# Kernel tuning notes

Measured on AMD Instinct MI355X. Metric: run time of the kernel, lower is better.

Reference implementation:

```python
import jax, jax.numpy as jnp
import numpy as np
from jax import lax

DIM = 256
HEADS = 8
C3 = DIM * 3 // 4  # 192
C1 = DIM // 4      # 64


def conv1x1(x, w):
    # x: [b,c,h,w], w: [o,c] (1x1 conv, no bias)
    return jnp.einsum('bchw,oc->bohw', x, w)


def dwconv3x3(x, w):
    # x: [b,c,h,w], w: [c,1,3,3] depthwise
    return lax.conv_general_dilated(
        x, w, window_strides=(1, 1), padding='SAME',
        feature_group_count=x.shape[1],
        dimension_numbers=('NCHW', 'OIHW', 'NCHW'))


def l2norm(x, eps=1e-12):
    # torch F.normalize: x / max(||x||, eps) along last dim
    n = jnp.sqrt(jnp.sum(x * x, axis=-1, keepdims=True))
    return x / jnp.maximum(n, eps)


def setup_inputs() -> dict:
    key = jax.random.key(0)
    ks = jax.random.split(key, 10)
    s = 0.02
    return {
        'x': jax.random.normal(ks[0], (4, DIM, 128, 128), jnp.float32),
        'k_v': jax.random.normal(ks[1], (4, 256), jnp.float32),
        'temperature': jnp.ones((HEADS, 1, 1), jnp.float32),
        'w_kR': jax.random.normal(ks[2], (C3, 192), jnp.float32) * s,
        'w_kI': jax.random.normal(ks[3], (C1, 64), jnp.float32) * s,
        'w_qR': jax.random.normal(ks[4], (DIM, C3), jnp.float32) * s,
        'w_qdw': jax.random.normal(ks[5], (DIM, 1, 3, 3), jnp.float32) * s,
        'w_kvI': jax.random.normal(ks[6], (2 * DIM, C1), jnp.float32) * s,
        'w_kvdw': jax.random.normal(ks[7], (2 * DIM, 1, 3, 3), jnp.float32) * s,
        'w_proj': jax.random.normal(ks[8], (DIM, DIM), jnp.float32) * s,
    }


def reference(x, k_v, temperature, w_kR, w_kI, w_qR, w_qdw, w_kvI, w_kvdw, w_proj):
    b, c, h, w = x.shape
    # FiLM-style modulation: x * kv + x
    kvr = (k_v[:, :192] @ w_kR.T)[:, :, None, None]  # [b, C3, 1, 1]
    kvi = (k_v[:, 192:] @ w_kI.T)[:, :, None, None]  # [b, C1, 1, 1]
    x_r = x[:, :C3] * kvr + x[:, :C3]
    x_i = x[:, C3:] * kvi + x[:, C3:]
    # QKV projections
    q = dwconv3x3(conv1x1(x_r, w_qR), w_qdw)          # [b, dim, h, w]
    kv = dwconv3x3(conv1x1(x_i, w_kvI), w_kvdw)       # [b, 2*dim, h, w]
    k, v = jnp.split(kv, 2, axis=1)
    hd = DIM // HEADS
    hw = h * w
    q = q.reshape(b, HEADS, hd, hw)
    k = k.reshape(b, HEADS, hd, hw)
    v = v.reshape(b, HEADS, hd, hw)
    # channel-wise (transposed) attention with L2 norm + temperature
    q = l2norm(q)
    k = l2norm(k)
    attn = jnp.einsum('bhcn,bhdn->bhcd', q, k) * temperature  # [b,H,hd,hd]
    attn = jax.nn.softmax(attn, axis=-1)
    out = jnp.einsum('bhcd,bhdn->bhcn', attn, v)
    out = out.reshape(b, DIM, h, w)
    return conv1x1(out, w_proj)
```

## Files before the change

kernel.cpp:

```cpp
#include <hip/hip_runtime.h>
#include <math.h>

#define HW 16384

typedef unsigned int uint;
typedef short bfrag __attribute__((ext_vector_type(8)));
typedef float f32x4 __attribute__((ext_vector_type(4)));

union FragCvt { uint4 u; bfrag v; };

__device__ inline uint pack2bf(float a, float b) {
  uint ua = __builtin_bit_cast(uint, a);
  uint ub = __builtin_bit_cast(uint, b);
  ua = (ua + 0x7FFFu + ((ua >> 16) & 1u)) >> 16;
  ub = (ub + 0x7FFFu + ((ub >> 16) & 1u)) & 0xFFFF0000u;
  return ua | ub;
}

__device__ inline void cvt_hilo(float4 a, float4 b, bfrag& hi, bfrag& lo) {
  float v0[8] = {a.x, a.y, a.z, a.w, b.x, b.y, b.z, b.w};
  uint hv[4], lv[4];
  #pragma unroll
  for (int i = 0; i < 4; ++i) {
    float x0 = v0[2 * i], x1 = v0[2 * i + 1];
    uint h = pack2bf(x0, x1);
    float h0 = __builtin_bit_cast(float, h << 16);
    float h1 = __builtin_bit_cast(float, h & 0xFFFF0000u);
    hv[i] = h;
    lv[i] = pack2bf(x0 - h0, x1 - h1);
  }
  FragCvt ch, cl;
  ch.u = make_uint4(hv[0], hv[1], hv[2], hv[3]);
  cl.u = make_uint4(lv[0], lv[1], lv[2], lv[3]);
  hi = ch.v;
  lo = cl.v;
}

__global__ __launch_bounds__(256) void mod_kernel(
    const float* __restrict__ kv, const float* __restrict__ wkR,
    const float* __restrict__ wkI, float* __restrict__ mod)
{
  int b = blockIdx.x;
  int c = threadIdx.x;
  const float* kvb = kv + b * 256;
  float s = 0.f;
  if (c < 192) {
    const float* wr = wkR + c * 192;
    for (int j = 0; j < 192; ++j) s += kvb[j] * wr[j];
  } else {
    const float* wi = wkI + (c - 192) * 64;
    for (int j = 0; j < 64; ++j) s += kvb[192 + j] * wi[j];
  }
  mod[b * 256 + c] = 1.f + s;
}

__global__ __launch_bounds__(256) void mgemm(
    const float* __restrict__ W, int ldW, size_t Wbstride,
    const float* __restrict__ X, int c0, size_t Xbstride,
    const float* __restrict__ mod,
    float* __restrict__ Y, size_t Ybstride, int K)
{
  int b = blockIdx.z, mt = blockIdx.y, nt = blockIdx.x;
  const float* Wb = W + (size_t)b * Wbstride + (size_t)mt * 128 * ldW;
  const float* Xb = X + (size_t)b * Xbstride + (size_t)c0 * HW + nt * 128;
  float* Yb = Y + (size_t)b * Ybstride + (size_t)mt * 128 * HW + nt * 128;

  __shared__ unsigned short Al[128 * 40];
  __shared__ unsigned short Bl[128 * 40];

  int t = threadIdx.x;
  int w = t >> 6, l = t & 63;
  int wm = (w >> 1) * 64, wn = (w & 1) * 64;
  int lm = l & 15, lk = (l >> 4) * 8;

  int am = t >> 1, ako = (t & 1) * 16;
  int bn = t & 127, bo = (t >> 7) * 8;

  f32x4 acc[4][4];
  #pragma unroll
  for (int fi = 0; fi < 4; ++fi)
    #pragma unroll
    for (int fj = 0; fj < 4; ++fj) acc[fi][fj] = {0.f, 0.f, 0.f, 0.f};

  for (int k0 = 0; k0 < K; k0 += 32) {
    const float* wsrc = Wb + (size_t)am * ldW + k0 + ako;
    float4 a0 = *(const float4*)(wsrc);
    float4 a1 = *(const float4*)(wsrc + 4);
    float4 a2 = *(const float4*)(wsrc + 8);
    float4 a3 = *(const float4*)(wsrc + 12);

    float xr[2][8];
    #pragma unroll
    for (int i = 0; i < 2; ++i) {
      int kb = k0 + bo + i * 16;
      #pragma unroll
      for (int r = 0; r < 8; ++r)
        xr[i][r] = Xb[(size_t)(kb + r) * HW + bn];
    }
    float sc[2][8];
    if (mod) {
      const float* mp = mod + b * 256 + c0 + k0 + bo;
      #pragma unroll
      for (int i = 0; i < 2; ++i) {
        float4 m0 = *(const float4*)(mp + i * 16);
        float4 m1 = *(const float4*)(mp + i * 16 + 4);
        sc[i][0] = m0.x; sc[i][1] = m0.y; sc[i][2] = m0.z; sc[i][3] = m0.w;
        sc[i][4] = m1.x; sc[i][5] = m1.y; sc[i][6] = m1.z; sc[i][7] = m1.w;
      }
    } else {
      #pragma unroll
      for (int i = 0; i < 2; ++i)
        #pragma unroll
        for (int r = 0; r < 8; ++r) sc[i][r] = 1.f;
    }

    __syncthreads();

    uint4 aw0, aw1;
    aw0.x = pack2bf(a0.x, a0.y); aw0.y = pack2bf(a0.z, a0.w);
    aw0.z = pack2bf(a1.x, a1.y); aw0.w = pack2bf(a1.z, a1.w);
    aw1.x = pack2bf(a2.x, a2.y); aw1.y = pack2bf(a2.z, a2.w);
    aw1.z = pack2bf(a3.x, a3.y); aw1.w = pack2bf(a3.z, a3.w);
    *(uint4*)&Al[am * 40 + ako] = aw0;
    *(uint4*)&Al[am * 40 + ako + 8] = aw1;

    #pragma unroll
    for (int i = 0; i < 2; ++i) {
      uint4 bw;
      bw.x = pack2bf(xr[i][0] * sc[i][0], xr[i][1] * sc[i][1]);
      bw.y = pack2bf(xr[i][2] * sc[i][2], xr[i][3] * sc[i][3]);
      bw.z = pack2bf(xr[i][4] * sc[i][4], xr[i][5] * sc[i][5]);
      bw.w = pack2bf(xr[i][6] * sc[i][6], xr[i][7] * sc[i][7]);
      *(uint4*)&Bl[bn * 40 + bo + i * 16] = bw;
    }

    __syncthreads();

    bfrag af[4], bfr[4];
    #pragma unroll
    for (int fj = 0; fj < 4; ++fj) {
      FragCvt cv;
      cv.u = *(const uint4*)&Al[(wm + fj * 16 + lm) * 40 + lk];
      af[fj] = cv.v;
    }
    #pragma unroll
    for (int fi = 0; fi < 4; ++fi) {
      FragCvt cv;
      cv.u = *(const uint4*)&Bl[(wn + fi * 16 + lm) * 40 + lk];
      bfr[fi] = cv.v;
    }
    #pragma unroll
    for (int fi = 0; fi < 4; ++fi)
      #pragma unroll
      for (int fj = 0; fj < 4; ++fj)
        acc[fi][fj] = __builtin_amdgcn_mfma_f32_16x16x32_bf16(
            bfr[fi], af[fj], acc[fi][fj], 0, 0, 0);
  }

  int ph = (l >> 4) * 4;
  #pragma unroll
  for (int fi = 0; fi < 4; ++fi)
    #pragma unroll
    for (int fj = 0; fj < 4; ++fj)
      *(f32x4*)&Yb[(size_t)(wm + fj * 16 + lm) * HW + wn + fi * 16 + ph] =
          acc[fi][fj];
}

__global__ __launch_bounds__(256) void dwconv_kernel(
    const float* __restrict__ in, size_t in_bstride,
    const float* __restrict__ wdw,
    float* __restrict__ out, size_t out_bstride,
    float* __restrict__ ssq)
{
  int c = blockIdx.x;
  int b = blockIdx.y;
  int t = threadIdx.x;
  int r = t >> 5;
  int xq = t & 31;

  const float4* ip4 = (const float4*)(in + (size_t)b * in_bstride + ((size_t)c << 14));
  float4* op4 = (float4*)(out + (size_t)b * out_bstride + ((size_t)c << 14));
  const float* wp = wdw + c * 9;
  float w0 = wp[0], w1 = wp[1], w2 = wp[2], w3 = wp[3], w4 = wp[4],
        w5 = wp[5], w6 = wp[6], w7 = wp[7], w8 = wp[8];

  const float4 z4 = make_float4(0.f, 0.f, 0.f, 0.f);
  int y0 = r << 4;

  float4 a = (y0 > 0) ? ip4[((y0 - 1) << 5) + xq] : z4;
  float4 bb = ip4[(y0 << 5) + xq];

  float aL = __shfl_up(a.w, 1);  if (xq == 0)  aL = 0.f;
  float aR = __shfl_down(a.x, 1); if (xq == 31) aR = 0.f;
  float bL = __shfl_up(bb.w, 1); if (xq == 0)  bL = 0.f;
  float bR = __shfl_down(bb.x, 1); if (xq == 31) bR = 0.f;

  float ss = 0.f;
  #pragma unroll
  for (int i = 0; i < 16; ++i) {
    int y = y0 + i;
    int yc = (y + 1 < 128) ? (y + 1) : 127;
    float4 cc = ip4[(yc << 5) + xq];
    if (y + 1 >= 128) { cc.x = 0.f; cc.y = 0.f; cc.z = 0.f; cc.w = 0.f; }
    float cL = __shfl_up(cc.w, 1);  if (xq == 0)  cL = 0.f;
    float cR = __shfl_down(cc.x, 1); if (xq == 31) cR = 0.f;

    float4 o;
    o.x = w0 * aL  + w1 * a.x + w2 * a.y +
          w3 * bL  + w4 * bb.x + w5 * bb.y +
          w6 * cL  + w7 * cc.x + w8 * cc.y;
    o.y = w0 * a.x + w1 * a.y + w2 * a.z +
          w3 * bb.x + w4 * bb.y + w5 * bb.z +
          w6 * cc.x + w7 * cc.y + w8 * cc.z;
    o.z = w0 * a.y + w1 * a.z + w2 * a.w +
          w3 * bb.y + w4 * bb.z + w5 * bb.w +
          w6 * cc.y + w7 * cc.z + w8 * cc.w;
    o.w = w0 * a.z + w1 * a.w + w2 * aR +
          w3 * bb.z + w4 * bb.w + w5 * bR +
          w6 * cc.z + w7 * cc.w + w8 * cR;

    op4[(y << 5) + xq] = o;
    ss += o.x * o.x + o.y * o.y + o.z * o.z + o.w * o.w;

    a = bb; aL = bL; aR = bR;
    bb = cc; bL = cL; bR = cR;
  }

  if (ssq) {
    #pragma unroll
    for (int off = 32; off > 0; off >>= 1) ss += __shfl_down(ss, off);
    __shared__ float red[4];
    if ((t & 63) == 0) red[t >> 6] = ss;
    __syncthreads();
    if (t == 0) ssq[b * 256 + c] = red[0] + red[1] + red[2] + red[3];
  }
}

__global__ __launch_bounds__(256) void gram_kernel(
    const float* __restrict__ qdw, const float* __restrict__ kdw,
    float* __restrict__ S)
{
  int chunk = blockIdx.x, h = blockIdx.y, b = blockIdx.z;
  int t = threadIdx.x;
  int w = t >> 6, l = t & 63;
  int lm = l & 15;
  int lk8 = (l >> 4) * 8;

  const float* qh = qdw + (((size_t)b * 256 + h * 32) << 14);
  const float* kh = kdw + (((size_t)b * 256 + h * 32) << 14);
  const float* q0 = qh + ((size_t)lm << 14);
  const float* q1 = q0 + ((size_t)16 << 14);
  const float* k0 = kh + ((size_t)lm << 14);
  const float* k1 = k0 + ((size_t)16 << 14);

  int px0 = chunk * 1024 + w * 256 + lk8;

  f32x4 acc[2][2], accl[2][2];
  #pragma unroll
  for (int mi = 0; mi < 2; ++mi)
    #pragma unroll
    for (int nj = 0; nj < 2; ++nj) {
      acc[mi][nj] = {0.f, 0.f, 0.f, 0.f};
      accl[mi][nj] = {0.f, 0.f, 0.f, 0.f};
    }

  #pragma unroll 2
  for (int s = 0; s < 8; ++s) {
    int px = px0 + s * 32;
    float4 a0 = *(const float4*)(q0 + px);
    float4 a1 = *(const float4*)(q0 + px + 4);
    float4 a2 = *(const float4*)(q1 + px);
    float4 a3 = *(const float4*)(q1 + px + 4);
    float4 b0 = *(const float4*)(k0 + px);
    float4 b1 = *(const float4*)(k0 + px + 4);
    float4 b2 = *(const float4*)(k1 + px);
    float4 b3 = *(const float4*)(k1 + px + 4);

    bfrag qhF[2], qlF[2], khF[2], klF[2];
    cvt_hilo(a0, a1, qhF[0], qlF[0]);
    cvt_hilo(a2, a3, qhF[1], qlF[1]);
    cvt_hilo(b0, b1, khF[0], klF[0]);
    cvt_hilo(b2, b3, khF[1], klF[1]);

    #pragma unroll
    for (int mi = 0; mi < 2; ++mi)
      #pragma unroll
      for (int nj = 0; nj < 2; ++nj) {
        acc[mi][nj] = __builtin_amdgcn_mfma_f32_16x16x32_bf16(
            qhF[mi], khF[nj], acc[mi][nj], 0, 0, 0);
        accl[mi][nj] = __builtin_amdgcn_mfma_f32_16x16x32_bf16(
            qhF[mi], klF[nj], accl[mi][nj], 0, 0, 0);
        accl[mi][nj] = __builtin_amdgcn_mfma_f32_16x16x32_bf16(
            qlF[mi], khF[nj], accl[mi][nj], 0, 0, 0);
      }
  }

  __shared__ float red[4][1024];
  int orow = (l >> 4) * 4;
  #pragma unroll
  for (int mi = 0; mi < 2; ++mi)
    #pragma unroll
    for (int nj = 0; nj < 2; ++nj)
      #pragma unroll
      for (int r = 0; r < 4; ++r)
        red[w][(mi * 16 + orow + r) * 32 + nj * 16 + lm] =
            acc[mi][nj][r] + accl[mi][nj][r];
  __syncthreads();
  float* Sp = S + (((size_t)b * 8 + h) << 10);
  for (int idx = t; idx < 1024; idx += 256)
    atomicAdd(&Sp[idx], red[0][idx] + red[1][idx] + red[2][idx] + red[3][idx]);
}

__global__ __launch_bounds__(64) void softmax_kernel(
    float* __restrict__ S, const float* __restrict__ ssq,
    const float* __restrict__ ssk, const float* __restrict__ temp)
{
  int bh = blockIdx.x;
  int b = bh >> 3, h = bh & 7;
  int c = threadIdx.x;
  if (c >= 32) return;
  float* row = S + ((size_t)bh << 10) + c * 32;
  float invq = 1.f / fmaxf(sqrtf(ssq[b * 256 + h * 32 + c]), 1e-12f);
  float T = temp[h];
  float lg[32];
  float mx = -1e30f;
  for (int d = 0; d < 32; ++d) {
    float invk = 1.f / fmaxf(sqrtf(ssk[b * 256 + h * 32 + d]), 1e-12f);
    float v = row[d] * invq * invk * T;
    lg[d] = v;
    mx = fmaxf(mx, v);
  }
  float sum = 0.f;
  for (int d = 0; d < 32; ++d) { float e = expf(lg[d] - mx); lg[d] = e; sum += e; }
  float inv = 1.f / sum;
  for (int d = 0; d < 32; ++d) row[d] = lg[d] * inv;
}

__global__ __launch_bounds__(256) void mbuild_kernel(
    const float* __restrict__ attn, const float* __restrict__ wproj,
    float* __restrict__ M)
{
  int o = blockIdx.x, b = blockIdx.y;
  int col = threadIdx.x;
  int h = col >> 5, d = col & 31;
  const float* a = attn + (((size_t)b * 8 + h) << 10);
  const float* wp = wproj + o * 256 + h * 32;
  float s = 0.f;
  #pragma unroll
  for (int cc = 0; cc < 32; ++cc) s += wp[cc] * a[cc * 32 + d];
  M[((size_t)b * 256 + o) * 256 + col] = s;
}

extern "C" void kernel_launch(void* const* d_in, const int* in_sizes, int n_in,
                              void* d_out, int out_size, void* d_ws, size_t ws_size,
                              hipStream_t stream)
{
  const float* x      = (const float*)d_in[0];
  const float* k_v    = (const float*)d_in[1];
  const float* temp   = (const float*)d_in[2];
  const float* w_kR   = (const float*)d_in[3];
  const float* w_kI   = (const float*)d_in[4];
  const float* w_qR   = (const float*)d_in[5];
  const float* w_qdw  = (const float*)d_in[6];
  const float* w_kvI  = (const float*)d_in[7];
  const float* w_kvdw = (const float*)d_in[8];
  const float* w_proj = (const float*)d_in[9];
  float* out = (float*)d_out;

  float* ws   = (float*)d_ws;
  float* bufA = ws;
  float* bufB = ws + 16777216;
  float* bufC = ws + 33554432;
  float* sm   = ws + 50331648;
  float* mod  = sm;
  float* ssq  = sm + 1024;
  float* ssk  = sm + 2048;
  float* S    = sm + 3072;
  float* M    = sm + 3072 + 32768;

  hipMemsetAsync(S, 0, (size_t)32768 * sizeof(float), stream);

  mod_kernel<<<dim3(4), dim3(256), 0, stream>>>(k_v, w_kR, w_kI, mod);

  mgemm<<<dim3(128, 2, 4), dim3(256), 0, stream>>>(
      w_kvI, 64, 0, x, 192, 4194304, mod, bufA, 4194304, 64);
  dwconv_kernel<<<dim3(256, 4), dim3(256), 0, stream>>>(
      bufA, 4194304, w_kvdw, bufB, 4194304, ssk);

  mgemm<<<dim3(128, 2, 4), dim3(256), 0, stream>>>(
      w_qR, 192, 0, x, 0, 4194304, mod, bufA, 4194304, 192);
  dwconv_kernel<<<dim3(256, 4), dim3(256), 0, stream>>>(
      bufA, 4194304, w_qdw, bufC, 4194304, ssq);

  gram_kernel<<<dim3(16, 8, 4), dim3(256), 0, stream>>>(bufC, bufB, S);

  mgemm<<<dim3(128, 2, 4), dim3(256), 0, stream>>>(
      w_kvI + 256 * 64, 64, 0, x, 192, 4194304, mod, bufA, 4194304, 64);

  softmax_kernel<<<dim3(32), dim3(64), 0, stream>>>(S, ssq, ssk, temp);
  mbuild_kernel<<<dim3(256, 4), dim3(256), 0, stream>>>(S, w_proj, M);

  dwconv_kernel<<<dim3(256, 4), dim3(256), 0, stream>>>(
      bufA, 4194304, w_kvdw + 256 * 9, bufC, 4194304, (float*)nullptr);

  mgemm<<<dim3(128, 2, 4), dim3(256), 0, stream>>>(
      M, 256, 65536, bufC, 0, 4194304, (const float*)nullptr, out, 4194304, 256);
}
```

Measured before the change: 337.2 us.

## Merge Q and K projection GEMMs into one launch, prefetch X tiles

```diff
diff --git a/kernel.cpp b/kernel.cpp
--- a/kernel.cpp
+++ b/kernel.cpp
@@ -54,21 +54,13 @@
   mod[b * 256 + c] = 1.f + s;
 }
 
-__global__ __launch_bounds__(256) void mgemm(
-    const float* __restrict__ W, int ldW, size_t Wbstride,
-    const float* __restrict__ X, int c0, size_t Xbstride,
-    const float* __restrict__ mod,
-    float* __restrict__ Y, size_t Ybstride, int K)
-{
-  int b = blockIdx.z, mt = blockIdx.y, nt = blockIdx.x;
-  const float* Wb = W + (size_t)b * Wbstride + (size_t)mt * 128 * ldW;
-  const float* Xb = X + (size_t)b * Xbstride + (size_t)c0 * HW + nt * 128;
-  float* Yb = Y + (size_t)b * Ybstride + (size_t)mt * 128 * HW + nt * 128;
-
-  __shared__ unsigned short Al[128 * 40];
-  __shared__ unsigned short Bl[128 * 40];
-
-  int t = threadIdx.x;
+__device__ __forceinline__ void mgemm_body(
+    const float* __restrict__ Wt, int ldW,
+    const float* __restrict__ Xt,
+    const float* __restrict__ modc,
+    float* __restrict__ Yt,
+    int K, int t, unsigned short* Al, unsigned short* Bl, float* Ml)
+{
   int w = t >> 6, l = t & 63;
   int wm = (w >> 1) * 64, wn = (w & 1) * 64;
   int lm = l & 15, lk = (l >> 4) * 8;
@@ -76,61 +68,54 @@
   int am = t >> 1, ako = (t & 1) * 16;
   int bn = t & 127, bo = (t >> 7) * 8;
 
+  Ml[t] = (modc && t < K) ? modc[t] : 1.f;
+
   f32x4 acc[4][4];
   #pragma unroll
   for (int fi = 0; fi < 4; ++fi)
     #pragma unroll
     for (int fj = 0; fj < 4; ++fj) acc[fi][fj] = {0.f, 0.f, 0.f, 0.f};
 
-  for (int k0 = 0; k0 < K; k0 += 32) {
-    const float* wsrc = Wb + (size_t)am * ldW + k0 + ako;
-    float4 a0 = *(const float4*)(wsrc);
-    float4 a1 = *(const float4*)(wsrc + 4);
-    float4 a2 = *(const float4*)(wsrc + 8);
-    float4 a3 = *(const float4*)(wsrc + 12);
-
-    float xr[2][8];
+  float xr[2][8];
+  auto load_x = [&](int k0) {
     #pragma unroll
     for (int i = 0; i < 2; ++i) {
       int kb = k0 + bo + i * 16;
       #pragma unroll
       for (int r = 0; r < 8; ++r)
-        xr[i][r] = Xb[(size_t)(kb + r) * HW + bn];
-    }
-    float sc[2][8];
-    if (mod) {
-      const float* mp = mod + b * 256 + c0 + k0 + bo;
-      #pragma unroll
-      for (int i = 0; i < 2; ++i) {
-        float4 m0 = *(const float4*)(mp + i * 16);
-        float4 m1 = *(const float4*)(mp + i * 16 + 4);
-        sc[i][0] = m0.x; sc[i][1] = m0.y; sc[i][2] = m0.z; sc[i][3] = m0.w;
-        sc[i][4] = m1.x; sc[i][5] = m1.y; sc[i][6] = m1.z; sc[i][7] = m1.w;
-      }
-    } else {
-      #pragma unroll
-      for (int i = 0; i < 2; ++i)
-        #pragma unroll
-        for (int r = 0; r < 8; ++r) sc[i][r] = 1.f;
-    }
-
+        xr[i][r] = Xt[(size_t)(kb + r) * HW + bn];
+    }
+  };
+
+  load_x(0);
+
+  for (int k0 = 0; k0 < K; k0 += 32) {
     __syncthreads();
 
-    uint4 aw0, aw1;
-    aw0.x = pack2bf(a0.x, a0.y); aw0.y = pack2bf(a0.z, a0.w);
-    aw0.z = pack2bf(a1.x, a1.y); aw0.w = pack2bf(a1.z, a1.w);
-    aw1.x = pack2bf(a2.x, a2.y); aw1.y = pack2bf(a2.z, a2.w);
-    aw1.z = pack2bf(a3.x, a3.y); aw1.w = pack2bf(a3.z, a3.w);
-    *(uint4*)&Al[am * 40 + ako] = aw0;
-    *(uint4*)&Al[am * 40 + ako + 8] = aw1;
+    {
+      const float* wsrc = Wt + (size_t)am * ldW + k0 + ako;
+      float4 a0 = *(const float4*)(wsrc);
+      float4 a1 = *(const float4*)(wsrc + 4);
+      float4 a2 = *(const float4*)(wsrc + 8);
+      float4 a3 = *(const float4*)(wsrc + 12);
+      uint4 aw0, aw1;
+      aw0.x = pack2bf(a0.x, a0.y); aw0.y = pack2bf(a0.z, a0.w);
+      aw0.z = pack2bf(a1.x, a1.y); aw0.w = pack2bf(a1.z, a1.w);
+      aw1.x = pack2bf(a2.x, a2.y); aw1.y = pack2bf(a2.z, a2.w);
+      aw1.z = pack2bf(a3.x, a3.y); aw1.w = pack2bf(a3.z, a3.w);
+      *(uint4*)&Al[am * 40 + ako] = aw0;
+      *(uint4*)&Al[am * 40 + ako + 8] = aw1;
+    }
 
     #pragma unroll
     for (int i = 0; i < 2; ++i) {
+      float4 m0 = *(const float4*)&Ml[k0 + bo + i * 16];
+      float4 m1 = *(const float4*)&Ml[k0 + bo + i * 16 + 4];
       uint4 bw;
-      bw.x = pack2bf(xr[i][0] * sc[i][0], xr[i][1] * sc[i][1]);
-      bw.y = pack2bf(xr[i][2] * sc[i][2], xr[i][3] * sc[i][3]);
-      bw.z = pack2bf(xr[i][4] * sc[i][4], xr[i][5] * sc[i][5]);
-      bw.w = pack2bf(xr[i][6] * sc[i][6], xr[i][7] * sc[i][7]);
+      bw.x = pack2bf(xr[i][0] * m0.x, xr[i][1] * m0.y);
+      bw.y = pack2bf(xr[i][2] * m0.z, xr[i][3] * m0.w);
+      bw.z = pack2bf(xr[i][4] * m1.x, xr[i][5] * m1.y);
+      bw.w = pack2bf(xr[i][6] * m1.z, xr[i][7] * m1.w);
       *(uint4*)&Bl[bn * 40 + bo + i * 16] = bw;
     }
 
@@ -149,6 +134,9 @@
       cv.u = *(const uint4*)&Bl[(wn + fi * 16 + lm) * 40 + lk];
       bfr[fi] = cv.v;
     }
+
+    if (k0 + 32 < K) load_x(k0 + 32);
+
     #pragma unroll
     for (int fi = 0; fi < 4; ++fi)
       #pragma unroll
@@ -162,8 +150,50 @@
   for (int fi = 0; fi < 4; ++fi)
     #pragma unroll
     for (int fj = 0; fj < 4; ++fj)
-      *(f32x4*)&Yb[(size_t)(wm + fj * 16 + lm) * HW + wn + fi * 16 + ph] =
+      *(f32x4*)&Yt[(size_t)(wm + fj * 16 + lm) * HW + wn + fi * 16 + ph] =
           acc[fi][fj];
+}
+
+__global__ __launch_bounds__(256, 4) void mgemm(
+    const float* __restrict__ W, int ldW, size_t Wbstride,
+    const float* __restrict__ X, int c0, size_t Xbstride,
+    const float* __restrict__ mod,
+    float* __restrict__ Y, size_t Ybstride, int K)
+{
+  __shared__ unsigned short Al[128 * 40];
+  __shared__ unsigned short Bl[128 * 40];
+  __shared__ float Ml[256];
+  int b = blockIdx.z, mt = blockIdx.y, nt = blockIdx.x;
+  mgemm_body(W + (size_t)b * Wbstride + (size_t)mt * 128 * ldW, ldW,
+             X + (size_t)b * Xbstride + (size_t)c0 * HW + nt * 128,
+             mod ? mod + b * 256 + c0 : (const float*)nullptr,
+             Y + (size_t)b * Ybstride + (size_t)mt * 128 * HW + nt * 128,
+             K, threadIdx.x, Al, Bl, Ml);
+}
+
+__global__ __launch_bounds__(256, 4) void mgemm_qk(
+    const float* __restrict__ wqR, const float* __restrict__ wkvI,
+    const float* __restrict__ X, const float* __restrict__ mod,
+    float* __restrict__ Yq, float* __restrict__ Yk)
+{
+  __shared__ unsigned short Al[128 * 40];
+  __shared__ unsigned short Bl[128 * 40];
+  __shared__ float Ml[256];
+  int b = blockIdx.z, mt = blockIdx.y, nt = blockIdx.x;
+  if (mt < 2) {
+    mgemm_body(wqR + (size_t)mt * 128 * 192, 192,
+               X + (size_t)b * 4194304 + nt * 128,
+               mod + b * 256,
+               Yq + (size_t)b * 4194304 + (size_t)mt * 128 * HW + nt * 128,
+               192, threadIdx.x, Al, Bl, Ml);
+  } else {
+    int m2 = mt - 2;
+    mgemm_body(wkvI + (size_t)m2 * 128 * 64, 64,
+               X + (size_t)b * 4194304 + (size_t)192 * HW + nt * 128,
+               mod + b * 256 + 192,
+               Yk + (size_t)b * 4194304 + (size_t)m2 * 128 * HW + nt * 128,
+               64, threadIdx.x, Al, Bl, Ml);
+  }
 }
 
 __global__ __launch_bounds__(256) void dwconv_kernel(
@@ -382,17 +412,16 @@
 
   mod_kernel<<<dim3(4), dim3(256), 0, stream>>>(k_v, w_kR, w_kI, mod);
 
-  mgemm<<<dim3(128, 2, 4), dim3(256), 0, stream>>>(
-      w_kvI, 64, 0, x, 192, 4194304, mod, bufA, 4194304, 64);
+  mgemm_qk<<<dim3(128, 4, 4), dim3(256), 0, stream>>>(
+      w_qR, w_kvI, x, mod, bufA, bufB);
+
   dwconv_kernel<<<dim3(256, 4), dim3(256), 0, stream>>>(
-      bufA, 4194304, w_kvdw, bufB, 4194304, ssk);
-
-  mgemm<<<dim3(128, 2, 4), dim3(256), 0, stream>>>(
-      w_qR, 192, 0, x, 0, 4194304, mod, bufA, 4194304, 192);
+      bufB, 4194304, w_kvdw, bufC, 4194304, ssk);
+
   dwconv_kernel<<<dim3(256, 4), dim3(256), 0, stream>>>(
-      bufA, 4194304, w_qdw, bufC, 4194304, ssq);
-
-  gram_kernel<<<dim3(16, 8, 4), dim3(256), 0, stream>>>(bufC, bufB, S);
+      bufA, 4194304, w_qdw, bufB, 4194304, ssq);
+
+  gram_kernel<<<dim3(16, 8, 4), dim3(256), 0, stream>>>(bufB, bufC, S);
 
   mgemm<<<dim3(128, 2, 4), dim3(256), 0, stream>>>(
       w_kvI + 256 * 64, 64, 0, x, 192, 4194304, mod, bufA, 4194304, 64);
```

New measurement: 321.8 us. 1.05x faster.
